# Optimization experiments

Hardware: AMD Instinct MI355X
Metric: run time of the kernel (lower is better)

The kernel has to match this reference:

```python
import jax, jax.numpy as jnp
import numpy as np

BATCH_SIZE = 4096
FPC = 8  # frames per camera
DIM = 256
EPS = 1e-8


def _build_indices(B, f):
    """Replicates distmtxidxlbl: for each block and each ordered pair (row, i)
    with row < i inside the block, the logit row gathers dist[row] at columns
    [0..blk) ++ [i] ++ [blk+f..B), and the label is blk (position of the
    positive i in that gathered row)."""
    base = np.arange(B)
    anchors, cols, labels = [], [], []
    for blk in range(0, B, f):
        rest = np.concatenate([base[:blk], base[blk + f:]])  # [B - f]
        for row in range(blk, blk + f):
            for i in range(row + 1, blk + f):
                anchors.append(row)
                cols.append(np.insert(rest, blk, i))  # [B - f + 1]
                labels.append(blk)
    return (np.asarray(anchors, np.int32),
            np.stack(cols).astype(np.int32),
            np.asarray(labels, np.int32))

ANCHORS, COLS, LABELS = _build_indices(BATCH_SIZE, FPC)  # [P], [P, L], [P]


def _euclidean_distance_matrix(x):
    # Standard stable pairwise Euclidean distance (Gram-matrix form) with
    # eps substitution at exact zeros, as in utils.euclidean_distance_matrix.
    dot = x @ x.T                                  # [B, B]
    sq = jnp.diagonal(dot)                         # [B]
    d2 = sq[None, :] - 2.0 * dot + sq[:, None]     # [B, B]
    d2 = jnp.maximum(d2, 0.0)
    zero = d2 == 0.0
    d = jnp.sqrt(jnp.where(zero, EPS, d2))
    return jnp.where(zero, 0.0, d)


def setup_inputs() -> dict:
    key = jax.random.key(0)
    x = jax.random.normal(key, (BATCH_SIZE, DIM), dtype=jnp.float32)
    return {"x": x}


def reference(x) -> jnp.ndarray:
    xs = jnp.squeeze(x)                                  # [B, D]
    dist = _euclidean_distance_matrix(xs)                # [B, B]
    anchors = jnp.asarray(ANCHORS)
    cols = jnp.asarray(COLS)
    labels = jnp.asarray(LABELS)
    logits = dist[anchors[:, None], cols]                # [P, L] gather
    logp = jax.nn.log_softmax(logits, axis=-1)           # [P, L]
    nll = -jnp.take_along_axis(logp, labels[:, None].astype(jnp.int32), axis=1)[:, 0]
    return jnp.mean(nll)
```

## Files before the change

kernel.cpp:

```cpp
#include <hip/hip_runtime.h>
#include <math.h>

#define BATCH 4096
#define DIM 256
#define FPC 8
#define NPAIR 14336
#define SHIFT 22.0f
#define NT 64
#define NTILE (NT * (NT + 1) / 2)

typedef __bf16 bf16x8 __attribute__((ext_vector_type(8)));
typedef float  f32x4  __attribute__((ext_vector_type(4)));

__device__ __forceinline__ unsigned short f2bf(float f) {
    unsigned int u = __float_as_uint(f);
    u += 0x7FFFu + ((u >> 16) & 1u);
    return (unsigned short)(u >> 16);
}

__device__ __forceinline__ void g2l16(const void* g, void* l) {
    __builtin_amdgcn_global_load_lds((__attribute__((address_space(1))) void*)(g),
                                     (__attribute__((address_space(3))) void*)(l),
                                     16, 0, 0);
}


__global__ __launch_bounds__(256) void prep_kernel(const float* __restrict__ x,
                                                   float* __restrict__ sq,
                                                   unsigned short* __restrict__ xb,
                                                   float* __restrict__ out) {
    int t = blockIdx.x * 256 + threadIdx.x;
    int row = t >> 6;
    int lane = t & 63;
    float4 v = ((const float4*)(x + row * DIM))[lane];
    ushort4 b;
    b.x = f2bf(v.x); b.y = f2bf(v.y); b.z = f2bf(v.z); b.w = f2bf(v.w);
    ((ushort4*)(xb + row * DIM))[lane] = b;
    float s = v.x * v.x + v.y * v.y + v.z * v.z + v.w * v.w;
#pragma unroll
    for (int off = 32; off > 0; off >>= 1) s += __shfl_xor(s, off);
    if (lane == 0) sq[row] = s;
    if (t == 0) out[0] = 0.f;
}

__global__ __launch_bounds__(256) void dist_expsum_mfma(const unsigned short* __restrict__ xb,
                                                        const float* __restrict__ sq,
                                                        float* __restrict__ P) {
    __shared__ unsigned short As[64][64];
    __shared__ unsigned short Bs[64][64];

    int t = blockIdx.x, bi = 0;
    while (t >= NT - bi) { t -= NT - bi; bi++; }
    const int bj = bi + t;
    const int row0 = bi * 64;
    const int col0 = bj * 64;
    const bool diagblk = (bi == bj);

    const int tid  = threadIdx.x;
    const int w    = tid >> 6;
    const int lane = tid & 63;
    const int wr   = w >> 1;
    const int wc   = w & 1;
    const int quad = lane >> 4;
    const int lcol = lane & 15;

    f32x4 acc[2][2];
#pragma unroll
    for (int i = 0; i < 2; i++)
#pragma unroll
        for (int j = 0; j < 2; j++) {
            f32x4 z = {0.f, 0.f, 0.f, 0.f};
            acc[i][j] = z;
        }

    const int swz = ((lane & 7) ^ (lane >> 3)) * 8;
    const int ldsoff = lane * 8;

    for (int ph = 0; ph < 4; ph++) {
        const int k0 = ph * 64;
        __syncthreads();
#pragma unroll
        for (int c = 0; c < 2; c++) {
            const int rb = w * 16 + c * 8;
            const int r  = rb + (lane >> 3);
            g2l16(xb + (size_t)(row0 + r) * DIM + k0 + swz,
                  (unsigned short*)&As[rb][0] + ldsoff);
            g2l16(xb + (size_t)(col0 + r) * DIM + k0 + swz,
                  (unsigned short*)&Bs[rb][0] + ldsoff);
        }
        __syncthreads();

#pragma unroll
        for (int kk = 0; kk < 2; kk++) {
            const int slot = ((kk * 4 + quad) ^ (lcol & 7)) * 8;
            bf16x8 a[2], b[2];
#pragma unroll
            for (int i = 0; i < 2; i++)
                a[i] = *(const bf16x8*)&As[wr * 32 + i * 16 + lcol][slot];
#pragma unroll
            for (int j = 0; j < 2; j++)
                b[j] = *(const bf16x8*)&Bs[wc * 32 + j * 16 + lcol][slot];
#pragma unroll
            for (int i = 0; i < 2; i++)
#pragma unroll
                for (int j = 0; j < 2; j++)
                    acc[i][j] = __builtin_amdgcn_mfma_f32_16x16x32_bf16(a[i], b[j], acc[i][j], 0, 0, 0);
        }
    }

    float sc2[2];
#pragma unroll
    for (int j = 0; j < 2; j++) sc2[j] = sq[col0 + wc * 32 + j * 16 + lcol];

    float cs[2] = {0.f, 0.f};
    const int rslot = 2 * bj + wc;
    const int cslot = 2 * bi + wr;

#pragma unroll
    for (int i = 0; i < 2; i++) {
        const int rbase = row0 + wr * 32 + i * 16 + quad * 4;
        const float4 s4 = *(const float4*)(sq + rbase);
        const float sr[4] = {s4.x, s4.y, s4.z, s4.w};
        float rs[4] = {0.f, 0.f, 0.f, 0.f};
#pragma unroll
        for (int j = 0; j < 2; j++) {
            const bool extile = diagblk && (wr * 2 + i == wc * 2 + j);
            float csj = 0.f;
#pragma unroll
            for (int r = 0; r < 4; r++) {
                float d2 = sr[r] + sc2[j] - 2.f * acc[i][j][r];
                float dd = sqrtf(fmaxf(d2, 0.f));
                float e = __expf(dd - SHIFT);
                if (extile && (((quad * 4 + r) >> 3) == (lcol >> 3))) e = 0.f;
                rs[r] += e;
                csj += e;
            }
            cs[j] += csj;
        }
#pragma unroll
        for (int m = 1; m < 16; m <<= 1) {
#pragma unroll
            for (int r = 0; r < 4; r++) rs[r] += __shfl_xor(rs[r], m);
        }
        if (lcol == 0) {
#pragma unroll
            for (int r = 0; r < 4; r++) P[(size_t)(rbase + r) * 128 + rslot] = rs[r];
        }
    }

    if (!diagblk) {
#pragma unroll
        for (int j = 0; j < 2; j++) {
            cs[j] += __shfl_xor(cs[j], 16);
            cs[j] += __shfl_xor(cs[j], 32);
        }
        if (lane < 16) {
#pragma unroll
            for (int j = 0; j < 2; j++)
                P[(size_t)(col0 + wc * 32 + j * 16 + lane) * 128 + cslot] = cs[j];
        }
    }
}

__global__ __launch_bounds__(256) void pairs_kernel(const float* __restrict__ x,
                                                    const float* __restrict__ P,
                                                    float* __restrict__ out) {
    __shared__ float Srow[FPC];
    __shared__ float wsum[4];
    const int tid = threadIdx.x;
    const int base = blockIdx.x * FPC;

    {
        const int rl  = tid >> 5;
        const int l32 = tid & 31;
        const float* pr = P + (size_t)(base + rl) * 128;
        float s2 = (pr[l32] + pr[32 + l32]) + (pr[64 + l32] + pr[96 + l32]);
#pragma unroll
        for (int m = 1; m < 32; m <<= 1) s2 += __shfl_xor(s2, m);
        if (l32 == 0) Srow[rl] = s2;
    }
    __syncthreads();

    const int p = tid >> 3;
    const int g = tid & 7;

    float nll = 0.f;
    if (p < 28) {
        int a = 0, q = p;
        while (q >= 7 - a) { q -= 7 - a; a++; }
        const int b = a + 1 + q;
        const float4* xa  = (const float4*)(x + (size_t)(base + a) * DIM);
        const float4* xbp = (const float4*)(x + (size_t)(base + b) * DIM);
        float d2 = 0.f;
#pragma unroll
        for (int r = 0; r < 8; r++) {
            float4 va = xa[r * 8 + g], vb = xbp[r * 8 + g];
            float dx = va.x - vb.x, dy = va.y - vb.y;
            float dz = va.z - vb.z, dw = va.w - vb.w;
            d2 = fmaf(dx, dx, d2); d2 = fmaf(dy, dy, d2);
            d2 = fmaf(dz, dz, d2); d2 = fmaf(dw, dw, d2);
        }
        d2 += __shfl_xor(d2, 1);
        d2 += __shfl_xor(d2, 2);
        d2 += __shfl_xor(d2, 4);
        if (g == 0) {
            float dd = sqrtf(fmaxf(d2, 0.f));
            nll = SHIFT + __logf(Srow[a] + __expf(dd - SHIFT)) - dd;
        }
    }
#pragma unroll
    for (int off = 1; off < 64; off <<= 1) nll += __shfl_xor(nll, off);
    if ((tid & 63) == 0) wsum[tid >> 6] = nll;
    __syncthreads();
    if (tid == 0)
        atomicAdd(out, (wsum[0] + wsum[1] + wsum[2] + wsum[3]) * (1.0f / (float)NPAIR));
}

extern "C" void kernel_launch(void* const* d_in, const int* in_sizes, int n_in,
                              void* d_out, int out_size, void* d_ws, size_t ws_size,
                              hipStream_t stream) {
    const float* x = (const float*)d_in[0];
    float* sq = (float*)d_ws;
    float* P  = sq + BATCH;
    unsigned short* xb = (unsigned short*)(P + (size_t)BATCH * 128);
    float* out = (float*)d_out;

    prep_kernel<<<BATCH * 64 / 256, 256, 0, stream>>>(x, sq, xb, out);

    dist_expsum_mfma<<<NTILE, 256, 0, stream>>>(xb, sq, P);

    pairs_kernel<<<BATCH / FPC, 256, 0, stream>>>(x, P, out);
}
```

Measured before the change: 82.53 us.

## Fuse prep, distance tiles and pair loss into one cooperative persistent kernel

Merges the three kernels into a single cooperative launch with grid-wide syncs between the prep, tile and pairs phases, using grid-stride loops over prep groups, triangular tiles and camera blocks. The aim is to remove two kernel launch boundaries and their gaps. In exchange it adds grid.sync overhead, calls an occupancy query on the host every launch, and gives the tile phase (2080 tiles) fewer resident blocks, which can leave work imbalanced. If the cooperative launch fails it falls back to the separate kernels.

```diff
diff --git a/kernel.cpp b/kernel.cpp
--- a/kernel.cpp
+++ b/kernel.cpp
@@ -1,5 +1,8 @@
 #include <hip/hip_runtime.h>
+#include <hip/hip_cooperative_groups.h>
 #include <math.h>
+
+namespace cg = cooperative_groups;
 
 #define BATCH 4096
 #define DIM 256
@@ -25,38 +28,39 @@
 }
 
 
-__global__ __launch_bounds__(256) void prep_kernel(const float* __restrict__ x,
-                                                   float* __restrict__ sq,
-                                                   unsigned short* __restrict__ xb,
-                                                   float* __restrict__ out) {
-    int t = blockIdx.x * 256 + threadIdx.x;
-    int row = t >> 6;
-    int lane = t & 63;
-    float4 v = ((const float4*)(x + row * DIM))[lane];
-    ushort4 b;
-    b.x = f2bf(v.x); b.y = f2bf(v.y); b.z = f2bf(v.z); b.w = f2bf(v.w);
-    ((ushort4*)(xb + row * DIM))[lane] = b;
-    float s = v.x * v.x + v.y * v.y + v.z * v.z + v.w * v.w;
-#pragma unroll
-    for (int off = 32; off > 0; off >>= 1) s += __shfl_xor(s, off);
-    if (lane == 0) sq[row] = s;
-    if (t == 0) out[0] = 0.f;
-}
-
-__global__ __launch_bounds__(256) void dist_expsum_mfma(const unsigned short* __restrict__ xb,
-                                                        const float* __restrict__ sq,
-                                                        float* __restrict__ P) {
-    __shared__ unsigned short As[64][64];
-    __shared__ unsigned short Bs[64][64];
-
-    int t = blockIdx.x, bi = 0;
+
+__device__ __forceinline__ void prep_body(int g, int tid, const float* __restrict__ x,
+                                          float* __restrict__ sq,
+                                          unsigned short* __restrict__ xb) {
+    const int row = g * FPC + (tid >> 5);
+    const int c   = tid & 31;
+    const float4* xr = (const float4*)(x + (size_t)row * DIM);
+    float4 v0 = xr[c], v1 = xr[c + 32];
+    ushort4 b0, b1;
+    b0.x = f2bf(v0.x); b0.y = f2bf(v0.y); b0.z = f2bf(v0.z); b0.w = f2bf(v0.w);
+    b1.x = f2bf(v1.x); b1.y = f2bf(v1.y); b1.z = f2bf(v1.z); b1.w = f2bf(v1.w);
+    ushort4* xo = (ushort4*)(xb + (size_t)row * DIM);
+    xo[c] = b0; xo[c + 32] = b1;
+    float s = v0.x * v0.x + v0.y * v0.y + v0.z * v0.z + v0.w * v0.w
+            + v1.x * v1.x + v1.y * v1.y + v1.z * v1.z + v1.w * v1.w;
+#pragma unroll
+    for (int m = 1; m < 32; m <<= 1) s += __shfl_xor(s, m);
+    if (c == 0) sq[row] = s;
+}
+
+__device__ __forceinline__ void tile_body(int tile, int tid,
+                                          const unsigned short* __restrict__ xb,
+                                          const float* __restrict__ sq,
+                                          float* __restrict__ P,
+                                          unsigned short (*As)[64],
+                                          unsigned short (*Bs)[64]) {
+    int t = tile, bi = 0;
     while (t >= NT - bi) { t -= NT - bi; bi++; }
     const int bj = bi + t;
     const int row0 = bi * 64;
     const int col0 = bj * 64;
     const bool diagblk = (bi == bj);
 
-    const int tid  = threadIdx.x;
     const int w    = tid >> 6;
     const int lane = tid & 63;
     const int wr   = w >> 1;
@@ -162,14 +166,10 @@
     }
 }
 
-__global__ __launch_bounds__(256) void pairs_kernel(const float* __restrict__ x,
-                                                    const float* __restrict__ P,
-                                                    float* __restrict__ out) {
-    __shared__ float Srow[FPC];
-    __shared__ float wsum[4];
-    const int tid = threadIdx.x;
-    const int base = blockIdx.x * FPC;
-
+__device__ __forceinline__ void pairs_body(int g, int tid, const float* __restrict__ x,
+                                           const float* __restrict__ P,
+                                           float* Sm, float* __restrict__ out) {
+    const int base = g * FPC;
     {
         const int rl  = tid >> 5;
         const int l32 = tid & 31;
@@ -177,13 +177,12 @@
         float s2 = (pr[l32] + pr[32 + l32]) + (pr[64 + l32] + pr[96 + l32]);
 #pragma unroll
         for (int m = 1; m < 32; m <<= 1) s2 += __shfl_xor(s2, m);
-        if (l32 == 0) Srow[rl] = s2;
+        if (l32 == 0) Sm[rl] = s2;
     }
     __syncthreads();
 
-    const int p = tid >> 3;
-    const int g = tid & 7;
-
+    const int p  = tid >> 3;
+    const int gg = tid & 7;
     float nll = 0.f;
     if (p < 28) {
         int a = 0, q = p;
@@ -194,7 +193,7 @@
         float d2 = 0.f;
 #pragma unroll
         for (int r = 0; r < 8; r++) {
-            float4 va = xa[r * 8 + g], vb = xbp[r * 8 + g];
+            float4 va = xa[r * 8 + gg], vb = xbp[r * 8 + gg];
             float dx = va.x - vb.x, dy = va.y - vb.y;
             float dz = va.z - vb.z, dw = va.w - vb.w;
             d2 = fmaf(dx, dx, d2); d2 = fmaf(dy, dy, d2);
@@ -203,17 +202,70 @@
         d2 += __shfl_xor(d2, 1);
         d2 += __shfl_xor(d2, 2);
         d2 += __shfl_xor(d2, 4);
-        if (g == 0) {
+        if (gg == 0) {
             float dd = sqrtf(fmaxf(d2, 0.f));
-            nll = SHIFT + __logf(Srow[a] + __expf(dd - SHIFT)) - dd;
+            nll = SHIFT + __logf(Sm[a] + __expf(dd - SHIFT)) - dd;
         }
     }
 #pragma unroll
     for (int off = 1; off < 64; off <<= 1) nll += __shfl_xor(nll, off);
-    if ((tid & 63) == 0) wsum[tid >> 6] = nll;
+    if ((tid & 63) == 0) Sm[8 + (tid >> 6)] = nll;
     __syncthreads();
     if (tid == 0)
-        atomicAdd(out, (wsum[0] + wsum[1] + wsum[2] + wsum[3]) * (1.0f / (float)NPAIR));
+        atomicAdd(out, (Sm[8] + Sm[9] + Sm[10] + Sm[11]) * (1.0f / (float)NPAIR));
+    __syncthreads();
+}
+
+
+__global__ __launch_bounds__(256) void fused_kernel(const float* __restrict__ x,
+                                                    float* __restrict__ sq,
+                                                    float* __restrict__ P,
+                                                    unsigned short* __restrict__ xb,
+                                                    float* __restrict__ out) {
+    __shared__ unsigned short As[64][64];
+    __shared__ unsigned short Bs[64][64];
+    __shared__ float Sm[16];
+
+    const int tid = threadIdx.x;
+    const int blk = blockIdx.x;
+    const int gsz = gridDim.x;
+
+    for (int g = blk; g < 512; g += gsz) prep_body(g, tid, x, sq, xb);
+    if (blk == 0 && tid == 0) out[0] = 0.f;
+
+    cg::this_grid().sync();
+
+    for (int tile = blk; tile < NTILE; tile += gsz)
+        tile_body(tile, tid, xb, sq, P, As, Bs);
+
+    cg::this_grid().sync();
+
+    for (int g = blk; g < 512; g += gsz) pairs_body(g, tid, x, P, Sm, out);
+}
+
+
+__global__ __launch_bounds__(256) void prep_kernel(const float* __restrict__ x,
+                                                   float* __restrict__ sq,
+                                                   unsigned short* __restrict__ xb,
+                                                   float* __restrict__ out) {
+    int t = blockIdx.x * 256 + threadIdx.x;
+    prep_body(t >> 8, threadIdx.x, x, sq, xb);
+    if (t == 0) out[0] = 0.f;
+}
+
+__global__ __launch_bounds__(256) void dist_kernel(const unsigned short* __restrict__ xb,
+                                                   const float* __restrict__ sq,
+                                                   float* __restrict__ P) {
+    __shared__ unsigned short As[64][64];
+    __shared__ unsigned short Bs[64][64];
+    tile_body(blockIdx.x, threadIdx.x, xb, sq, P, As, Bs);
+}
+
+__global__ __launch_bounds__(256) void pairs_kernel(const float* __restrict__ x,
+                                                    const float* __restrict__ P,
+                                                    float* __restrict__ out) {
+    __shared__ float Sm[16];
+    pairs_body(blockIdx.x, threadIdx.x, x, P, Sm, out);
 }
 
 extern "C" void kernel_launch(void* const* d_in, const int* in_sizes, int n_in,
@@ -225,9 +277,21 @@
     unsigned short* xb = (unsigned short*)(P + (size_t)BATCH * 128);
     float* out = (float*)d_out;
 
-    prep_kernel<<<BATCH * 64 / 256, 256, 0, stream>>>(x, sq, xb, out);
-
-    dist_expsum_mfma<<<NTILE, 256, 0, stream>>>(xb, sq, P);
-
-    pairs_kernel<<<BATCH / FPC, 256, 0, stream>>>(x, P, out);
-}
+    int perCU = 0;
+    hipError_t oerr = hipOccupancyMaxActiveBlocksPerMultiprocessor(
+        &perCU, fused_kernel, 256, 0);
+    int grid = 1024;
+    if (oerr == hipSuccess && perCU > 0) {
+        int cap = perCU * 256;
+        if (cap < grid) grid = cap;
+    }
+
+    void* args[] = { (void*)&x, (void*)&sq, (void*)&P, (void*)&xb, (void*)&out };
+    hipError_t lerr = hipLaunchCooperativeKernel((void*)fused_kernel, dim3(grid),
+                                                 dim3(256), args, 0, stream);
+    if (lerr != hipSuccess) {
+        prep_kernel<<<512, 256, 0, stream>>>(x, sq, xb, out);
+        dist_kernel<<<NTILE, 256, 0, stream>>>(xb, sq, P);
+        pairs_kernel<<<512, 256, 0, stream>>>(x, P, out);
+    }
+}
```

New measurement: 201.6 us. 2.44x slower.

## Fuse bf16 conversion and squared-norm prep into the MFMA distance kernel

Applied to the files above, without the earlier changes.

Removes the separate prep kernel. Each distance tile block now loads fp32 rows of x directly, converts them to bf16 in registers, writes them into swizzled LDS, and accumulates the row squared norms locally. This saves one kernel launch and the round trip of the bf16 copy and the norms through global memory. In exchange, every tile re-reads and re-converts fp32 data (twice the bytes of bf16), and the async global-to-LDS loads become register-staged stores. The norms are now computed from fp32 per tile instead of once per row.

```diff
diff --git a/kernel.cpp b/kernel.cpp
--- a/kernel.cpp
+++ b/kernel.cpp
@@ -18,36 +18,22 @@
     return (unsigned short)(u >> 16);
 }
 
-__device__ __forceinline__ void g2l16(const void* g, void* l) {
-    __builtin_amdgcn_global_load_lds((__attribute__((address_space(1))) void*)(g),
-                                     (__attribute__((address_space(3))) void*)(l),
-                                     16, 0, 0);
-}
-
-
-__global__ __launch_bounds__(256) void prep_kernel(const float* __restrict__ x,
-                                                   float* __restrict__ sq,
-                                                   unsigned short* __restrict__ xb,
+__device__ __forceinline__ unsigned pk2(float lo, float hi) {
+    return ((unsigned)f2bf(hi) << 16) | (unsigned)f2bf(lo);
+}
+
+__device__ __forceinline__ float dot4(float4 v) {
+    return v.x * v.x + v.y * v.y + v.z * v.z + v.w * v.w;
+}
+
+
+__global__ __launch_bounds__(256) void dist_kernel(const float* __restrict__ x,
+                                                   float* __restrict__ P,
                                                    float* __restrict__ out) {
-    int t = blockIdx.x * 256 + threadIdx.x;
-    int row = t >> 6;
-    int lane = t & 63;
-    float4 v = ((const float4*)(x + row * DIM))[lane];
-    ushort4 b;
-    b.x = f2bf(v.x); b.y = f2bf(v.y); b.z = f2bf(v.z); b.w = f2bf(v.w);
-    ((ushort4*)(xb + row * DIM))[lane] = b;
-    float s = v.x * v.x + v.y * v.y + v.z * v.z + v.w * v.w;
-#pragma unroll
-    for (int off = 32; off > 0; off >>= 1) s += __shfl_xor(s, off);
-    if (lane == 0) sq[row] = s;
-    if (t == 0) out[0] = 0.f;
-}
-
-__global__ __launch_bounds__(256) void dist_expsum_mfma(const unsigned short* __restrict__ xb,
-                                                        const float* __restrict__ sq,
-                                                        float* __restrict__ P) {
     __shared__ unsigned short As[64][64];
     __shared__ unsigned short Bs[64][64];
+    __shared__ float sqA[64];
+    __shared__ float sqB[64];
 
     int t = blockIdx.x, bi = 0;
     while (t >= NT - bi) { t -= NT - bi; bi++; }
@@ -56,7 +42,9 @@
     const int col0 = bj * 64;
     const bool diagblk = (bi == bj);
 
-    const int tid  = threadIdx.x;
+    const int tid = threadIdx.x;
+    if (blockIdx.x == 0 && tid == 0) out[0] = 0.f;
+
     const int w    = tid >> 6;
     const int lane = tid & 63;
     const int wr   = w >> 1;
@@ -64,6 +52,13 @@
     const int quad = lane >> 4;
     const int lcol = lane & 15;
 
+    const int rr = tid >> 2;
+    const int gg = tid & 3;
+    const int s0 = ((gg * 2)     ^ (rr & 7)) * 8;
+    const int s1 = ((gg * 2 + 1) ^ (rr & 7)) * 8;
+    const float4* pa = (const float4*)(x + (size_t)(row0 + rr) * DIM + gg * 16);
+    const float4* pb = (const float4*)(x + (size_t)(col0 + rr) * DIM + gg * 16);
+
     f32x4 acc[2][2];
 #pragma unroll
     for (int i = 0; i < 2; i++)
@@ -73,21 +68,34 @@
             acc[i][j] = z;
         }
 
-    const int swz = ((lane & 7) ^ (lane >> 3)) * 8;
-    const int ldsoff = lane * 8;
-
+    float ssA = 0.f, ssB = 0.f;
+
+#pragma unroll
     for (int ph = 0; ph < 4; ph++) {
-        const int k0 = ph * 64;
+        const int k4 = ph * 16;
+        float4 a0 = pa[k4], a1 = pa[k4 + 1], a2 = pa[k4 + 2], a3 = pa[k4 + 3];
+        float4 b0 = pb[k4], b1 = pb[k4 + 1], b2 = pb[k4 + 2], b3 = pb[k4 + 3];
+
         __syncthreads();
-#pragma unroll
-        for (int c = 0; c < 2; c++) {
-            const int rb = w * 16 + c * 8;
-            const int r  = rb + (lane >> 3);
-            g2l16(xb + (size_t)(row0 + r) * DIM + k0 + swz,
-                  (unsigned short*)&As[rb][0] + ldsoff);
-            g2l16(xb + (size_t)(col0 + r) * DIM + k0 + swz,
-                  (unsigned short*)&Bs[rb][0] + ldsoff);
-        }
+
+        uint4 wA0, wA1, wB0, wB1;
+        wA0.x = pk2(a0.x, a0.y); wA0.y = pk2(a0.z, a0.w);
+        wA0.z = pk2(a1.x, a1.y); wA0.w = pk2(a1.z, a1.w);
+        wA1.x = pk2(a2.x, a2.y); wA1.y = pk2(a2.z, a2.w);
+        wA1.z = pk2(a3.x, a3.y); wA1.w = pk2(a3.z, a3.w);
+        wB0.x = pk2(b0.x, b0.y); wB0.y = pk2(b0.z, b0.w);
+        wB0.z = pk2(b1.x, b1.y); wB0.w = pk2(b1.z, b1.w);
+        wB1.x = pk2(b2.x, b2.y); wB1.y = pk2(b2.z, b2.w);
+        wB1.z = pk2(b3.x, b3.y); wB1.w = pk2(b3.z, b3.w);
+
+        *(uint4*)((unsigned short*)&As[rr][0] + s0) = wA0;
+        *(uint4*)((unsigned short*)&As[rr][0] + s1) = wA1;
+        *(uint4*)((unsigned short*)&Bs[rr][0] + s0) = wB0;
+        *(uint4*)((unsigned short*)&Bs[rr][0] + s1) = wB1;
+
+        ssA += dot4(a0) + dot4(a1) + dot4(a2) + dot4(a3);
+        ssB += dot4(b0) + dot4(b1) + dot4(b2) + dot4(b3);
+
         __syncthreads();
 
 #pragma unroll
@@ -108,9 +116,14 @@
         }
     }
 
+    ssA += __shfl_xor(ssA, 1); ssA += __shfl_xor(ssA, 2);
+    ssB += __shfl_xor(ssB, 1); ssB += __shfl_xor(ssB, 2);
+    if (gg == 0) { sqA[rr] = ssA; sqB[rr] = ssB; }
+    __syncthreads();
+
     float sc2[2];
 #pragma unroll
-    for (int j = 0; j < 2; j++) sc2[j] = sq[col0 + wc * 32 + j * 16 + lcol];
+    for (int j = 0; j < 2; j++) sc2[j] = sqB[wc * 32 + j * 16 + lcol];
 
     float cs[2] = {0.f, 0.f};
     const int rslot = 2 * bj + wc;
@@ -118,9 +131,9 @@
 
 #pragma unroll
     for (int i = 0; i < 2; i++) {
-        const int rbase = row0 + wr * 32 + i * 16 + quad * 4;
-        const float4 s4 = *(const float4*)(sq + rbase);
-        const float sr[4] = {s4.x, s4.y, s4.z, s4.w};
+        const int lr0 = wr * 32 + i * 16 + quad * 4;
+        const int rbase = row0 + lr0;
+        const float sr[4] = {sqA[lr0], sqA[lr0 + 1], sqA[lr0 + 2], sqA[lr0 + 3]};
         float rs[4] = {0.f, 0.f, 0.f, 0.f};
 #pragma unroll
         for (int j = 0; j < 2; j++) {
@@ -220,14 +233,9 @@
                               void* d_out, int out_size, void* d_ws, size_t ws_size,
                               hipStream_t stream) {
     const float* x = (const float*)d_in[0];
-    float* sq = (float*)d_ws;
-    float* P  = sq + BATCH;
-    unsigned short* xb = (unsigned short*)(P + (size_t)BATCH * 128);
+    float* P = (float*)d_ws;
     float* out = (float*)d_out;
 
-    prep_kernel<<<BATCH * 64 / 256, 256, 0, stream>>>(x, sq, xb, out);
-
-    dist_expsum_mfma<<<NTILE, 256, 0, stream>>>(xb, sq, P);
-
+    dist_kernel<<<NTILE, 256, 0, stream>>>(x, P, out);
     pairs_kernel<<<BATCH / FPC, 256, 0, stream>>>(x, P, out);
 }
```

New measurement: 88.67 us. 7.4% more time.

## Double-buffer LDS tiles and process two upper-triangle tiles per block

Applied to the files above, without the earlier changes.

The distance/exp-sum kernel now loads the next K-slice into a second LDS buffer while MFMAs run on the current one, removing the load-sync-compute serialization. Each block also handles two 64x64 tiles (grid 1040 instead of 2080), so the prefetch carries over into the second tile and launch overhead is amortized. This doubles LDS use and halves the block count, which may reduce latency hiding through occupancy on a 256-CU part.

```diff
diff --git a/kernel.cpp b/kernel.cpp
--- a/kernel.cpp
+++ b/kernel.cpp
@@ -8,6 +8,7 @@
 #define SHIFT 22.0f
 #define NT 64
 #define NTILE (NT * (NT + 1) / 2)
+#define GRID_D 1040
 
 typedef __bf16 bf16x8 __attribute__((ext_vector_type(8)));
 typedef float  f32x4  __attribute__((ext_vector_type(4)));
@@ -43,18 +44,11 @@
     if (t == 0) out[0] = 0.f;
 }
 
-__global__ __launch_bounds__(256) void dist_expsum_mfma(const unsigned short* __restrict__ xb,
-                                                        const float* __restrict__ sq,
-                                                        float* __restrict__ P) {
-    __shared__ unsigned short As[64][64];
-    __shared__ unsigned short Bs[64][64];
-
-    int t = blockIdx.x, bi = 0;
-    while (t >= NT - bi) { t -= NT - bi; bi++; }
-    const int bj = bi + t;
-    const int row0 = bi * 64;
-    const int col0 = bj * 64;
-    const bool diagblk = (bi == bj);
+__global__ __launch_bounds__(256) void dist_kernel(const unsigned short* __restrict__ xb,
+                                                   const float* __restrict__ sq,
+                                                   float* __restrict__ P) {
+    __shared__ unsigned short As[2][64][64];
+    __shared__ unsigned short Bs[2][64][64];
 
     const int tid  = threadIdx.x;
     const int w    = tid >> 6;
@@ -64,6 +58,18 @@
     const int quad = lane >> 4;
     const int lcol = lane & 15;
 
+    const int swz = ((lane & 7) ^ (lane >> 3)) * 8;
+    const int ldsoff = lane * 8;
+    const int srow = lane >> 3;
+
+    int bi_[2], bj_[2];
+#pragma unroll
+    for (int k = 0; k < 2; k++) {
+        int t = blockIdx.x + k * GRID_D, bi = 0;
+        while (t >= NT - bi) { t -= NT - bi; bi++; }
+        bi_[k] = bi; bj_[k] = bi + t;
+    }
+
     f32x4 acc[2][2];
 #pragma unroll
     for (int i = 0; i < 2; i++)
@@ -73,22 +79,39 @@
             acc[i][j] = z;
         }
 
-    const int swz = ((lane & 7) ^ (lane >> 3)) * 8;
-    const int ldsoff = lane * 8;
-
-    for (int ph = 0; ph < 4; ph++) {
-        const int k0 = ph * 64;
-        __syncthreads();
+    {
+        const int row0 = bi_[0] * 64, col0 = bj_[0] * 64;
 #pragma unroll
         for (int c = 0; c < 2; c++) {
             const int rb = w * 16 + c * 8;
-            const int r  = rb + (lane >> 3);
-            g2l16(xb + (size_t)(row0 + r) * DIM + k0 + swz,
-                  (unsigned short*)&As[rb][0] + ldsoff);
-            g2l16(xb + (size_t)(col0 + r) * DIM + k0 + swz,
-                  (unsigned short*)&Bs[rb][0] + ldsoff);
-        }
+            const int r  = rb + srow;
+            g2l16(xb + (size_t)(row0 + r) * DIM + swz,
+                  (unsigned short*)&As[0][rb][0] + ldsoff);
+            g2l16(xb + (size_t)(col0 + r) * DIM + swz,
+                  (unsigned short*)&Bs[0][rb][0] + ldsoff);
+        }
+    }
+
+    for (int q = 0; q < 8; q++) {
+        const int buf = q & 1;
         __syncthreads();
+
+        if (q < 7) {
+            const int qn = q + 1;
+            const int tn = qn >> 2;
+            const int row0n = bi_[tn] * 64;
+            const int col0n = bj_[tn] * 64;
+            const int k0n = (qn & 3) * 64;
+#pragma unroll
+            for (int c = 0; c < 2; c++) {
+                const int rb = w * 16 + c * 8;
+                const int r  = rb + srow;
+                g2l16(xb + (size_t)(row0n + r) * DIM + k0n + swz,
+                      (unsigned short*)&As[buf ^ 1][rb][0] + ldsoff);
+                g2l16(xb + (size_t)(col0n + r) * DIM + k0n + swz,
+                      (unsigned short*)&Bs[buf ^ 1][rb][0] + ldsoff);
+            }
+        }
 
 #pragma unroll
         for (int kk = 0; kk < 2; kk++) {
@@ -96,68 +119,84 @@
             bf16x8 a[2], b[2];
 #pragma unroll
             for (int i = 0; i < 2; i++)
-                a[i] = *(const bf16x8*)&As[wr * 32 + i * 16 + lcol][slot];
+                a[i] = *(const bf16x8*)&As[buf][wr * 32 + i * 16 + lcol][slot];
 #pragma unroll
             for (int j = 0; j < 2; j++)
-                b[j] = *(const bf16x8*)&Bs[wc * 32 + j * 16 + lcol][slot];
+                b[j] = *(const bf16x8*)&Bs[buf][wc * 32 + j * 16 + lcol][slot];
 #pragma unroll
             for (int i = 0; i < 2; i++)
 #pragma unroll
                 for (int j = 0; j < 2; j++)
                     acc[i][j] = __builtin_amdgcn_mfma_f32_16x16x32_bf16(a[i], b[j], acc[i][j], 0, 0, 0);
         }
-    }
-
-    float sc2[2];
-#pragma unroll
-    for (int j = 0; j < 2; j++) sc2[j] = sq[col0 + wc * 32 + j * 16 + lcol];
-
-    float cs[2] = {0.f, 0.f};
-    const int rslot = 2 * bj + wc;
-    const int cslot = 2 * bi + wr;
-
-#pragma unroll
-    for (int i = 0; i < 2; i++) {
-        const int rbase = row0 + wr * 32 + i * 16 + quad * 4;
-        const float4 s4 = *(const float4*)(sq + rbase);
-        const float sr[4] = {s4.x, s4.y, s4.z, s4.w};
-        float rs[4] = {0.f, 0.f, 0.f, 0.f};
-#pragma unroll
-        for (int j = 0; j < 2; j++) {
-            const bool extile = diagblk && (wr * 2 + i == wc * 2 + j);
-            float csj = 0.f;
-#pragma unroll
-            for (int r = 0; r < 4; r++) {
-                float d2 = sr[r] + sc2[j] - 2.f * acc[i][j][r];
-                float dd = sqrtf(fmaxf(d2, 0.f));
-                float e = __expf(dd - SHIFT);
-                if (extile && (((quad * 4 + r) >> 3) == (lcol >> 3))) e = 0.f;
-                rs[r] += e;
-                csj += e;
+
+        if ((q & 3) == 3) {
+            const int tc = q >> 2;
+            const int bi = bi_[tc], bj = bj_[tc];
+            const int row0 = bi * 64, col0 = bj * 64;
+            const bool diagblk = (bi == bj);
+
+            float sc2[2];
+#pragma unroll
+            for (int j = 0; j < 2; j++) sc2[j] = sq[col0 + wc * 32 + j * 16 + lcol];
+
+            float cs[2] = {0.f, 0.f};
+            const int rslot = 2 * bj + wc;
+            const int cslot = 2 * bi + wr;
+
+#pragma unroll
+            for (int i = 0; i < 2; i++) {
+                const int rbase = row0 + wr * 32 + i * 16 + quad * 4;
+                const float4 s4 = *(const float4*)(sq + rbase);
+                const float sr[4] = {s4.x, s4.y, s4.z, s4.w};
+                float rs[4] = {0.f, 0.f, 0.f, 0.f};
+#pragma unroll
+                for (int j = 0; j < 2; j++) {
+                    const bool extile = diagblk && (wr * 2 + i == wc * 2 + j);
+                    float csj = 0.f;
+#pragma unroll
+                    for (int r = 0; r < 4; r++) {
+                        float d2 = sr[r] + sc2[j] - 2.f * acc[i][j][r];
+                        float dd = sqrtf(fmaxf(d2, 0.f));
+                        float e = __expf(dd - SHIFT);
+                        if (extile && (((quad * 4 + r) >> 3) == (lcol >> 3))) e = 0.f;
+                        rs[r] += e;
+                        csj += e;
+                    }
+                    cs[j] += csj;
+                }
+#pragma unroll
+                for (int m = 1; m < 16; m <<= 1) {
+#pragma unroll
+                    for (int r = 0; r < 4; r++) rs[r] += __shfl_xor(rs[r], m);
+                }
+                if (lcol == 0) {
+#pragma unroll
+                    for (int r = 0; r < 4; r++)
+                        P[(size_t)(rbase + r) * 128 + rslot] = rs[r];
+                }
             }
-            cs[j] += csj;
-        }
-#pragma unroll
-        for (int m = 1; m < 16; m <<= 1) {
-#pragma unroll
-            for (int r = 0; r < 4; r++) rs[r] += __shfl_xor(rs[r], m);
-        }
-        if (lcol == 0) {
-#pragma unroll
-            for (int r = 0; r < 4; r++) P[(size_t)(rbase + r) * 128 + rslot] = rs[r];
-        }
-    }
-
-    if (!diagblk) {
-#pragma unroll
-        for (int j = 0; j < 2; j++) {
-            cs[j] += __shfl_xor(cs[j], 16);
-            cs[j] += __shfl_xor(cs[j], 32);
-        }
-        if (lane < 16) {
-#pragma unroll
-            for (int j = 0; j < 2; j++)
-                P[(size_t)(col0 + wc * 32 + j * 16 + lane) * 128 + cslot] = cs[j];
+
+            if (!diagblk) {
+#pragma unroll
+                for (int j = 0; j < 2; j++) {
+                    cs[j] += __shfl_xor(cs[j], 16);
+                    cs[j] += __shfl_xor(cs[j], 32);
+                }
+                if (lane < 16) {
+#pragma unroll
+                    for (int j = 0; j < 2; j++)
+                        P[(size_t)(col0 + wc * 32 + j * 16 + lane) * 128 + cslot] = cs[j];
+                }
+            }
+
+#pragma unroll
+            for (int i = 0; i < 2; i++)
+#pragma unroll
+                for (int j = 0; j < 2; j++) {
+                    f32x4 z = {0.f, 0.f, 0.f, 0.f};
+                    acc[i][j] = z;
+                }
         }
     }
 }
@@ -227,7 +266,7 @@
 
     prep_kernel<<<BATCH * 64 / 256, 256, 0, stream>>>(x, sq, xb, out);
 
-    dist_expsum_mfma<<<NTILE, 256, 0, stream>>>(xb, sq, P);
+    dist_kernel<<<GRID_D, 256, 0, stream>>>(xb, sq, P);
 
     pairs_kernel<<<BATCH / FPC, 256, 0, stream>>>(x, P, out);
 }
```

New measurement: 87.57 us. 1.06x slower.
